# Kernel optimization log

Measured on AMD Instinct MI355X. Metric: run time of the kernel, lower is better.

## Reference

```python
import jax, jax.numpy as jnp
import numpy as np

B, S = 256, 256          # batch, seq_len
V, E = 8000, 128         # char vocab, char emb dim
HC, HW = 128, 256        # char_lstm_hid_dim, word_lstm_hid_dim


def setup_inputs() -> dict:
    key = jax.random.key(0)
    ks = jax.random.split(key, 20)
    n = lambda k, sh: (jax.random.normal(k, sh) * 0.05).astype(jnp.float32)
    return {
        "insts": jax.random.randint(ks[0], (B, S), 0, V),
        "golds": jax.random.randint(ks[1], (B, S), 0, 3),
        "emb": n(ks[2], (V, E)),
        "Wih_f": n(ks[3], (4 * HC, E)), "Whh_f": n(ks[4], (4 * HC, HC)), "b_f": n(ks[5], (4 * HC,)),
        "Wih_b": n(ks[6], (4 * HC, E)), "Whh_b": n(ks[7], (4 * HC, HC)), "b_b": n(ks[8], (4 * HC,)),
        "sub_Wih": n(ks[9], (4 * HW, 2 * HC)), "sub_Whh": n(ks[10], (4 * HW, HW)), "sub_b": n(ks[11], (4 * HW,)),
        "wrd_Wih": n(ks[12], (4 * HW, HW)), "wrd_Whh": n(ks[13], (4 * HW, HW)), "wrd_b": n(ks[14], (4 * HW,)),
        "cls_W": n(ks[15], (2, HW + 2 * HC)), "cls_b": n(ks[16], (2,)),
    }


def _cell(x, h, c, Wih, Whh, b):
    # PyTorch LSTMCell convention: gates ordered i, f, g, o
    g = x @ Wih.T + h @ Whh.T + b
    i, f, gg, o = jnp.split(g, 4, axis=-1)
    c = jax.nn.sigmoid(f) * c + jax.nn.sigmoid(i) * jnp.tanh(gg)
    h = jax.nn.sigmoid(o) * jnp.tanh(c)
    return h, c


def reference(insts, golds, emb, Wih_f, Whh_f, b_f, Wih_b, Whh_b, b_b,
              sub_Wih, sub_Whh, sub_b, wrd_Wih, wrd_Whh, wrd_b, cls_W, cls_b):
    # --- CharEncoder: embedding + BiLSTM, seq-first output [S, B, 2*HC] ---
    x = emb[insts].transpose(1, 0, 2)  # [S, B, E]
    z = jnp.zeros((B, HC), x.dtype)

    def mk_step(Wih, Whh, b):
        def step(hc, xt):
            h, c = _cell(xt, hc[0], hc[1], Wih, Whh, b)
            return (h, c), h
        return step

    _, hf = jax.lax.scan(mk_step(Wih_f, Whh_f, b_f), (z, z), x)
    _, hb = jax.lax.scan(mk_step(Wih_b, Whh_b, b_b), (z, z), x[::-1])
    chars = jnp.concatenate([hf, hb[::-1]], axis=-1)  # [S, B, 2*HC]

    # subword LSTM input at step t is chars[t-1] (zeros at t=0)
    sub_in = jnp.concatenate([jnp.zeros((1, B, 2 * HC), chars.dtype), chars[:-1]], axis=0)

    smap = jnp.array([1, 2, 2], jnp.int32)  # subword_action_map
    wmap = jnp.array([0, 1, 1], jnp.int32)  # word_action_map
    bidx = jnp.arange(B)

    # stacks: read state at pos, write new state at pos+1, then pos += op
    sh = jnp.zeros((2 * S + 2, B, HW), chars.dtype)
    sc = jnp.zeros((2 * S + 2, B, HW), chars.dtype)
    wh = jnp.zeros((S + 1, B, HW), chars.dtype)
    wc = jnp.zeros((S + 1, B, HW), chars.dtype)
    sp = jnp.zeros((B,), jnp.int32)
    wp = jnp.zeros((B,), jnp.int32)

    def step(carry, inp):
        sh, sc, sp, wh, wc, wp = carry
        xs, xc, g = inp  # subword input [B,2HC], classifier char feat [B,2HC], gold op [B]
        h1, c1 = _cell(xs, sh[sp, bidx], sc[sp, bidx], sub_Wih, sub_Whh, sub_b)
        sh = sh.at[sp + 1, bidx].set(h1)
        sc = sc.at[sp + 1, bidx].set(c1)
        h2, c2 = _cell(h1, wh[wp, bidx], wc[wp, bidx], wrd_Wih, wrd_Whh, wrd_b)
        wh = wh.at[wp + 1, bidx].set(h2)
        wc = wc.at[wp + 1, bidx].set(c2)
        out = jnp.concatenate([h2, xc], axis=-1) @ cls_W.T + cls_b  # [B, 2]
        return (sh, sc, sp + smap[g], wh, wc, wp + wmap[g]), out

    _, outs = jax.lax.scan(step, (sh, sc, sp, wh, wc, wp),
                           (sub_in, chars, golds.T.astype(jnp.int32)))
    return outs.transpose(1, 0, 2)  # [B, S, 2]
```

## Files before the change

### kernel.cpp

```cpp
#include <hip/hip_runtime.h>

#define S_LEN 256
#define BATCH 256

typedef _Float16 f16;
typedef _Float16 f16x8 __attribute__((ext_vector_type(8)));
typedef _Float16 f16x4 __attribute__((ext_vector_type(4)));
typedef float f32x4 __attribute__((ext_vector_type(4)));
typedef unsigned u32x4 __attribute__((ext_vector_type(4)));

__device__ inline float sigf(float x) { return 1.f / (1.f + __expf(-x)); }
__device__ inline float tanhf2(float x) { return 2.f * sigf(2.f * x) - 1.f; }

#define BARRIER_LGKM() asm volatile("s_waitcnt lgkmcnt(0)\n\ts_barrier" ::: "memory")

__global__ void k_convert(const float* __restrict__ w3, const float* __restrict__ w4,
                          const float* __restrict__ w6, const float* __restrict__ w7,
                          const float* __restrict__ w9, const float* __restrict__ w10,
                          const float* __restrict__ w12, const float* __restrict__ w13,
                          f16* __restrict__ dst) {
  int i = blockIdx.x * blockDim.x + threadIdx.x;
  const int n = 1310720;
  for (; i < n; i += gridDim.x * blockDim.x) {
    float v;
    if (i < 262144) {
      int m = i >> 16, j = i & 65535;
      v = (m == 0 ? w3 : m == 1 ? w4 : m == 2 ? w6 : w7)[j];
    } else {
      int k = i - 262144;
      int m = k >> 18, j = k & 262143;
      v = (m == 0 ? w9 : m == 1 ? w10 : m == 2 ? w12 : w13)[j];
    }
    dst[i] = (f16)v;
  }
}

__global__ void k_zero(unsigned* __restrict__ p, int n) {
  int i = blockIdx.x * blockDim.x + threadIdx.x;
  for (; i < n; i += gridDim.x * blockDim.x) p[i] = 0u;
}

__global__ void k_gather(const int* __restrict__ insts, const float* __restrict__ emb,
                         f16* __restrict__ Xf) {
  int gid = blockIdx.x * blockDim.x + threadIdx.x;
  int row = gid >> 5;
  int ch = gid & 31;
  int t = row >> 8, b = row & 255;
  int v = insts[b * S_LEN + t];
  const float* src = emb + (size_t)v * 128 + ch * 4;
  f16x4 d;
  d[0] = (f16)src[0]; d[1] = (f16)src[1]; d[2] = (f16)src[2]; d[3] = (f16)src[3];
  *(f16x4*)&Xf[(size_t)row * 128 + ch * 4] = d;
}

__global__ __launch_bounds__(512, 2)
void k_char_fused(const f16* __restrict__ wbuf, const float* __restrict__ bias_f,
                  const float* __restrict__ bias_b, const f16* __restrict__ Xf,
                  f16* __restrict__ chars) {
  const int dr = blockIdx.x >> 6;
  const int slice = blockIdx.x & 63;
  const int teamc = slice >> 2;
  const f16* Wih = wbuf + (dr ? 131072 : 0);
  const f16* Whh = wbuf + (dr ? 196608 : 65536);
  const float* bias = dr ? bias_b : bias_f;
  const int tid = threadIdx.x, lane = tid & 63, wave = tid >> 6;
  const int l15 = lane & 15, kb = (lane >> 4) * 8;
  const int bq = lane >> 4;
  const int u0 = wave * 16;
  const int cbase = dr ? 128 : 0;
  const int xrow = (slice * 4 + l15 < 256) ? (slice * 4 + l15) : 255;

  __shared__ f16 hs[2][16][136];
  __shared__ float gex[4][512];

  f16x8 fw[4][4], fh[4][4];
  float bv[4];
#pragma unroll
  for (int g = 0; g < 4; ++g) {
    const int row = g * 128 + u0 + l15;
    bv[g] = bias[row];
#pragma unroll
    for (int ks = 0; ks < 4; ++ks) {
      fw[g][ks] = *(const f16x8*)&Wih[row * 128 + ks * 32 + kb];
      fh[g][ks] = *(const f16x8*)&Whh[row * 128 + ks * 32 + kb];
    }
  }

  for (int i = tid; i < 2 * 16 * 136; i += 512) ((f16*)hs)[i] = (f16)0.f;
  __syncthreads();

  const int cb = tid >> 7;
  const int cu = tid & 127;
  float c = 0.f;

  f32x4 gacc[4];
  {
    const int t0 = dr ? 255 : 0;
    f16x8 ax[4];
#pragma unroll
    for (int ks = 0; ks < 4; ++ks)
      ax[ks] = *(const f16x8*)&Xf[(size_t)t0 * BATCH * 128 + xrow * 128 + ks * 32 + kb];
#pragma unroll
    for (int g = 0; g < 4; ++g) { f32x4 a = {bv[g], bv[g], bv[g], bv[g]}; gacc[g] = a; }
#pragma unroll
    for (int ks = 0; ks < 4; ++ks)
#pragma unroll
      for (int g = 0; g < 4; ++g)
        gacc[g] = __builtin_amdgcn_mfma_f32_16x16x32_f16(ax[ks], fw[g][ks], gacc[g], 0, 0, 0);
  }

  int par = 0;
  for (int st = 0; st < 256; ++st) {
    f16x8 axn[4];
    if (st < 255) {
      const int tn = dr ? (254 - st) : (st + 1);
#pragma unroll
      for (int ks = 0; ks < 4; ++ks)
        axn[ks] = *(const f16x8*)&Xf[(size_t)tn * BATCH * 128 + xrow * 128 + ks * 32 + kb];
    }

    f16x8 ah[4];
#pragma unroll
    for (int ks = 0; ks < 4; ++ks) ah[ks] = *(const f16x8*)&hs[par][l15][ks * 32 + kb];
    f32x4 acc[4];
#pragma unroll
    for (int g = 0; g < 4; ++g) acc[g] = gacc[g];
#pragma unroll
    for (int ks = 0; ks < 4; ++ks)
#pragma unroll
      for (int g = 0; g < 4; ++g)
        acc[g] = __builtin_amdgcn_mfma_f32_16x16x32_f16(ah[ks], fh[g][ks], acc[g], 0, 0, 0);

    if (bq == 0) {
#pragma unroll
      for (int g = 0; g < 4; ++g)
#pragma unroll
        for (int r = 0; r < 4; ++r) gex[r][g * 128 + u0 + l15] = acc[g][r];
    }
    BARRIER_LGKM();

    {
      float gi = gex[cb][cu], gf = gex[cb][128 + cu], gg = gex[cb][256 + cu],
            go = gex[cb][384 + cu];
      float cc = sigf(gf) * c + sigf(gi) * tanhf2(gg);
      c = cc;
      f16 hv = (f16)(sigf(go) * tanhf2(cc));
      const int t_out = dr ? (255 - st) : st;
      const int gr = slice * 4 + cb;
      chars[((size_t)(teamc * 256 + t_out) * 16 + (gr & 15)) * 256 + cbase + cu] = hv;
      hs[par ^ 1][cb][cu] = hv;
    }

    if (st < 255) {
#pragma unroll
      for (int g = 0; g < 4; ++g) { f32x4 a = {bv[g], bv[g], bv[g], bv[g]}; gacc[g] = a; }
#pragma unroll
      for (int ks = 0; ks < 4; ++ks)
#pragma unroll
        for (int g = 0; g < 4; ++g)
          gacc[g] =
              __builtin_amdgcn_mfma_f32_16x16x32_f16(axn[ks], fw[g][ks], gacc[g], 0, 0, 0);
    }
    par ^= 1;
    BARRIER_LGKM();
  }
}

__global__ __launch_bounds__(256, 1)
void k_subword(const f16* __restrict__ wbuf, const f16* __restrict__ chars,
               const int* __restrict__ golds,
               const float* __restrict__ b_sub, const float* __restrict__ b_wrd,
               unsigned* __restrict__ pub, unsigned* __restrict__ flags,
               f16* __restrict__ H2) {
  const int team = blockIdx.x >> 4;
  const int q = blockIdx.x & 15;
  const int m0 = team * 16;
  const int h0 = q * 16;
  const int tid = threadIdx.x, lane = tid & 63, wave = tid >> 6;
  const int l15 = lane & 15, kb = (lane >> 4) * 8;

  const f16* sWih = wbuf + 262144;
  const f16* sWhh = wbuf + 524288;
  const f16* wWih = wbuf + 786432;
  const f16* wWhh = wbuf + 1048576;

  __shared__ f16 xs_s[16][264];
  __shared__ f16 h1_s[16][264];
  __shared__ f16 wh_s[16][264];
  __shared__ float gexS[16][68];
  __shared__ float gexW[16][68];
  __shared__ int golds_s[16][256];

  f32x4 fsi[8], fsh[8], fwi[8], fwh[8];
  const int wr = wave * 256 + h0 + l15;
#pragma unroll
  for (int ks = 0; ks < 8; ++ks) {
    fsi[ks] = *(const volatile f32x4*)&sWih[wr * 256 + ks * 32 + kb];
    fsh[ks] = *(const volatile f32x4*)&sWhh[wr * 256 + ks * 32 + kb];
    fwi[ks] = *(const volatile f32x4*)&wWih[wr * 256 + ks * 32 + kb];
    fwh[ks] = *(const volatile f32x4*)&wWhh[wr * 256 + ks * 32 + kb];
  }
  const float bS = b_sub[wr], bW = b_wrd[wr];

  for (int i = tid; i < 16 * 256; i += 256)
    golds_s[i >> 8][i & 255] = golds[(m0 + (i >> 8)) * S_LEN + (i & 255)];
  for (int i = tid; i < 16 * 264; i += 256) {
    ((f16*)xs_s)[i] = (f16)0.f;
    ((f16*)h1_s)[i] = (f16)0.f;
    ((f16*)wh_s)[i] = (f16)0.f;
  }
  const int cm = tid >> 4, cj = tid & 15;
  const int sr = tid >> 4;
  const int sc = (tid & 15) * 16;
  float c_sub = 0.f, c_wrd = 0.f, wh_reg = 0.f;
  __syncthreads();

  for (int i = 0; i <= S_LEN; ++i) {
    const bool doW = (i > 0), doS = (i < S_LEN);
    const int slotbase = ((i & 1) * 16 + team) << 12;

    f16x4 chpre[4];
    if (doS) {
#pragma unroll
      for (int p = 0; p < 4; ++p)
        chpre[p] = *(const f16x4*)&chars[(size_t)(((team * S_LEN + i) * 16 + sr) * 256) +
                                         sc + p * 4];
    }

    f32x4 accW = {bW, bW, bW, bW};
    f32x4 accS = {bS, bS, bS, bS};
    if (doW) {
#pragma unroll
      for (int ks = 0; ks < 8; ++ks) {
        f16x8 a1 = *(const f16x8*)&h1_s[l15][ks * 32 + kb];
        f16x8 aw = *(const f16x8*)&wh_s[l15][ks * 32 + kb];
        accW = __builtin_amdgcn_mfma_f32_16x16x32_f16(
            a1, __builtin_bit_cast(f16x8, fwi[ks]), accW, 0, 0, 0);
        accW = __builtin_amdgcn_mfma_f32_16x16x32_f16(
            aw, __builtin_bit_cast(f16x8, fwh[ks]), accW, 0, 0, 0);
      }
    }
    if (doS) {
      const bool keep = (i > 0) && (golds_s[l15][i > 0 ? i - 1 : 0] == 0);
      f16x8 z8 = {};
#pragma unroll
      for (int ks = 0; ks < 8; ++ks) {
        f16x8 axv = *(const f16x8*)&xs_s[l15][ks * 32 + kb];
        f16x8 a1 = *(const f16x8*)&h1_s[l15][ks * 32 + kb];
        a1 = keep ? a1 : z8;
        accS = __builtin_amdgcn_mfma_f32_16x16x32_f16(
            axv, __builtin_bit_cast(f16x8, fsi[ks]), accS, 0, 0, 0);
        accS = __builtin_amdgcn_mfma_f32_16x16x32_f16(
            a1, __builtin_bit_cast(f16x8, fsh[ks]), accS, 0, 0, 0);
      }
    }
#pragma unroll
    for (int r = 0; r < 4; ++r) {
      if (doW) gexW[(lane >> 4) * 4 + r][wave * 16 + l15] = accW[r];
      if (doS) gexS[(lane >> 4) * 4 + r][wave * 16 + l15] = accS[r];
    }
    __syncthreads();

    const int gprev = (i > 0) ? golds_s[cm][i - 1] : 1;
    if (doW) {
      float gi = gexW[cm][cj], gf = gexW[cm][16 + cj], gg = gexW[cm][32 + cj],
            go = gexW[cm][48 + cj];
      float c2 = sigf(gf) * c_wrd + sigf(gi) * tanhf2(gg);
      float h2 = sigf(go) * tanhf2(c2);
      bool adv = (gprev != 0);
      if (adv) { c_wrd = c2; wh_reg = h2; }
      H2[(size_t)(i - 1) * BATCH * 256 + (m0 + cm) * 256 + h0 + cj] = (f16)h2;
    }
    if (doS) {
      float gi = gexS[cm][cj], gf = gexS[cm][16 + cj], gg = gexS[cm][32 + cj],
            go = gexS[cm][48 + cj];
      float cp = (gprev == 0) ? c_sub : 0.f;
      float c1 = sigf(gf) * cp + sigf(gi) * tanhf2(gg);
      c_sub = c1;
      f16 h1 = (f16)(sigf(go) * tanhf2(c1));
      unsigned val = ((unsigned)__builtin_bit_cast(unsigned short, h1) << 16) |
                     (unsigned)__builtin_bit_cast(unsigned short, (f16)wh_reg);
      __hip_atomic_store(&pub[slotbase + cm * 256 + h0 + cj], val, __ATOMIC_RELAXED,
                         __HIP_MEMORY_SCOPE_AGENT);
    }
    __syncthreads();

    if (doS) {
      if (tid == 0)
        __hip_atomic_store(&flags[(team * 16 + q) * 16], (unsigned)(i + 1), __ATOMIC_RELAXED,
                           __HIP_MEMORY_SCOPE_AGENT);
      if (tid < 64) {
        const unsigned tgt = (unsigned)(i + 1);
        while (true) {
          unsigned v = tgt;
          if (lane < 16)
            v = __hip_atomic_load(&flags[(team * 16 + lane) * 16], __ATOMIC_RELAXED,
                                  __HIP_MEMORY_SCOPE_AGENT);
          if (__all(v >= tgt)) break;
          __builtin_amdgcn_s_sleep(1);
        }
      }
      asm volatile("" ::: "memory");
      __syncthreads();
      u32x4 w0, w1, w2, w3;
      {
        const unsigned* pb = &pub[slotbase + sr * 256 + sc];
        asm volatile(
            "global_load_dwordx4 %0, %4, off sc0 sc1\n\t"
            "global_load_dwordx4 %1, %5, off sc0 sc1\n\t"
            "global_load_dwordx4 %2, %6, off sc0 sc1\n\t"
            "global_load_dwordx4 %3, %7, off sc0 sc1\n\t"
            "s_waitcnt vmcnt(0)"
            : "=&v"(w0), "=&v"(w1), "=&v"(w2), "=&v"(w3)
            : "v"(pb), "v"(pb + 4), "v"(pb + 8), "v"(pb + 12));
      }
      union { unsigned short s[8]; f16x8 v; } uh0, uw0, uh1, uw1;
#pragma unroll
      for (int k = 0; k < 4; ++k) {
        uh0.s[k] = (unsigned short)(w0[k] >> 16);
        uw0.s[k] = (unsigned short)(w0[k] & 0xffffu);
        uh0.s[4 + k] = (unsigned short)(w1[k] >> 16);
        uw0.s[4 + k] = (unsigned short)(w1[k] & 0xffffu);
        uh1.s[k] = (unsigned short)(w2[k] >> 16);
        uw1.s[k] = (unsigned short)(w2[k] & 0xffffu);
        uh1.s[4 + k] = (unsigned short)(w3[k] >> 16);
        uw1.s[4 + k] = (unsigned short)(w3[k] & 0xffffu);
      }
      *(f16x8*)&h1_s[sr][sc] = uh0.v;
      *(f16x8*)&wh_s[sr][sc] = uw0.v;
      *(f16x8*)&h1_s[sr][sc + 8] = uh1.v;
      *(f16x8*)&wh_s[sr][sc + 8] = uw1.v;
#pragma unroll
      for (int p = 0; p < 4; ++p) *(f16x4*)&xs_s[sr][sc + p * 4] = chpre[p];
      __syncthreads();
    }
  }
}

__global__ __launch_bounds__(256)
void k_cls(const f16* __restrict__ H2, const f16* __restrict__ chars,
           const float* __restrict__ clsW, const float* __restrict__ clsb,
           float* __restrict__ out) {
  const int w = (blockIdx.x << 2) | (threadIdx.x >> 6);
  const int lane = threadIdx.x & 63;
  const int t = w >> 8, b = w & 255;
  const f16* h2p = H2 + (size_t)w * 256;
  const f16* chp = chars + (size_t)(((b >> 4) * S_LEN + t) * 16 + (b & 15)) * 256;
  float s0 = 0.f, s1 = 0.f;
  f16x4 hv = *(const f16x4*)&h2p[lane * 4];
  f16x4 cv = *(const f16x4*)&chp[lane * 4];
#pragma unroll
  for (int qq = 0; qq < 4; ++qq) {
    int u = lane * 4 + qq;
    s0 += (float)hv[qq] * clsW[u] + (float)cv[qq] * clsW[256 + u];
    s1 += (float)hv[qq] * clsW[512 + u] + (float)cv[qq] * clsW[768 + u];
  }
#pragma unroll
  for (int off = 32; off >= 1; off >>= 1) {
    s0 += __shfl_down(s0, off);
    s1 += __shfl_down(s1, off);
  }
  if (lane == 0) {
    out[((size_t)b * S_LEN + t) * 2 + 0] = s0 + clsb[0];
    out[((size_t)b * S_LEN + t) * 2 + 1] = s1 + clsb[1];
  }
}

extern "C" void kernel_launch(void* const* d_in, const int* in_sizes, int n_in,
                              void* d_out, int out_size, void* d_ws, size_t ws_size,
                              hipStream_t stream) {
  const int* insts = (const int*)d_in[0];
  const int* golds = (const int*)d_in[1];
  const float* emb = (const float*)d_in[2];
  const float* wihf = (const float*)d_in[3];
  const float* whhf = (const float*)d_in[4];
  const float* bf = (const float*)d_in[5];
  const float* wihb = (const float*)d_in[6];
  const float* whhb = (const float*)d_in[7];
  const float* bb = (const float*)d_in[8];
  const float* swih = (const float*)d_in[9];
  const float* swhh = (const float*)d_in[10];
  const float* sb = (const float*)d_in[11];
  const float* wwih = (const float*)d_in[12];
  const float* wwhh = (const float*)d_in[13];
  const float* wb = (const float*)d_in[14];
  const float* clsW = (const float*)d_in[15];
  const float* clsb = (const float*)d_in[16];
  float* out = (float*)d_out;

  const size_t OFF_W = 0;
  const size_t OFF_XF = 2621440;
  const size_t OFF_PUB = OFF_XF + 4194304;
  const size_t OFF_FLAGS = OFF_PUB + 524288;
  const size_t OFF_CHARS = 19398656;
  const size_t OFF_A = 52953088;
  const size_t TOTAL = 87048192;
  if (ws_size < TOTAL) return;

  char* ws = (char*)d_ws;
  f16* wbuf = (f16*)(ws + OFF_W);
  f16* Xf = (f16*)(ws + OFF_XF);
  f16* chars = (f16*)(ws + OFF_CHARS);
  f16* H2 = (f16*)(ws + OFF_A);
  unsigned* pub = (unsigned*)(ws + OFF_PUB);
  unsigned* flags = (unsigned*)(ws + OFF_FLAGS);

  hipLaunchKernelGGL(k_convert, dim3(1024), dim3(256), 0, stream, wihf, whhf, wihb, whhb,
                     swih, swhh, wwih, wwhh, wbuf);
  hipLaunchKernelGGL(k_gather, dim3(8192), dim3(256), 0, stream, insts, emb, Xf);

  hipLaunchKernelGGL(k_char_fused, dim3(128), dim3(512), 0, stream, wbuf, bf, bb, Xf, chars);

  hipLaunchKernelGGL(k_zero, dim3(16), dim3(256), 0, stream, (unsigned*)(ws + OFF_FLAGS),
                     4096);
  hipLaunchKernelGGL(k_subword, dim3(256), dim3(256), 0, stream, wbuf, chars, golds, sb, wb,
                     pub, flags, H2);
  hipLaunchKernelGGL(k_cls, dim3(16384), dim3(256), 0, stream, H2, chars, clsW, clsb, out);
}
```

Baseline: 1.207 ms.

## Tag published subword state with step number and prefetch before flag spin

```diff
diff --git a/kernel.cpp b/kernel.cpp
--- a/kernel.cpp
+++ b/kernel.cpp
@@ -170,7 +170,7 @@
 void k_subword(const f16* __restrict__ wbuf, const f16* __restrict__ chars,
                const int* __restrict__ golds,
                const float* __restrict__ b_sub, const float* __restrict__ b_wrd,
-               unsigned* __restrict__ pub, unsigned* __restrict__ flags,
+               unsigned long long* __restrict__ pub, unsigned* __restrict__ flags,
                f16* __restrict__ H2) {
   const int team = blockIdx.x >> 4;
   const int q = blockIdx.x & 15;
@@ -278,8 +278,9 @@
       float c1 = sigf(gf) * cp + sigf(gi) * tanhf2(gg);
       c_sub = c1;
       f16 h1 = (f16)(sigf(go) * tanhf2(c1));
-      unsigned val = ((unsigned)__builtin_bit_cast(unsigned short, h1) << 16) |
-                     (unsigned)__builtin_bit_cast(unsigned short, (f16)wh_reg);
+      unsigned data = ((unsigned)__builtin_bit_cast(unsigned short, h1) << 16) |
+                      (unsigned)__builtin_bit_cast(unsigned short, (f16)wh_reg);
+      unsigned long long val = ((unsigned long long)(i + 1) << 32) | (unsigned long long)data;
       __hip_atomic_store(&pub[slotbase + cm * 256 + h0 + cj], val, __ATOMIC_RELAXED,
                          __HIP_MEMORY_SCOPE_AGENT);
     }
@@ -289,6 +290,21 @@
       if (tid == 0)
         __hip_atomic_store(&flags[(team * 16 + q) * 16], (unsigned)(i + 1), __ATOMIC_RELAXED,
                            __HIP_MEMORY_SCOPE_AGENT);
+      u32x4 w0, w1, w2, w3, w4, w5, w6, w7;
+      const unsigned long long* pb = &pub[slotbase + sr * 256 + sc];
+      asm volatile(
+          "global_load_dwordx4 %0, %8, off sc0 sc1\n\t"
+          "global_load_dwordx4 %1, %9, off sc0 sc1\n\t"
+          "global_load_dwordx4 %2, %10, off sc0 sc1\n\t"
+          "global_load_dwordx4 %3, %11, off sc0 sc1\n\t"
+          "global_load_dwordx4 %4, %12, off sc0 sc1\n\t"
+          "global_load_dwordx4 %5, %13, off sc0 sc1\n\t"
+          "global_load_dwordx4 %6, %14, off sc0 sc1\n\t"
+          "global_load_dwordx4 %7, %15, off sc0 sc1"
+          : "=&v"(w0), "=&v"(w1), "=&v"(w2), "=&v"(w3), "=&v"(w4), "=&v"(w5), "=&v"(w6),
+            "=&v"(w7)
+          : "v"(pb), "v"(pb + 2), "v"(pb + 4), "v"(pb + 6), "v"(pb + 8), "v"(pb + 10),
+            "v"(pb + 12), "v"(pb + 14));
       if (tid < 64) {
         const unsigned tgt = (unsigned)(i + 1);
         while (true) {
@@ -302,30 +318,44 @@
       }
       asm volatile("" ::: "memory");
       __syncthreads();
-      u32x4 w0, w1, w2, w3;
+      asm volatile("s_waitcnt vmcnt(0)"
+                   : "+v"(w0), "+v"(w1), "+v"(w2), "+v"(w3), "+v"(w4), "+v"(w5), "+v"(w6),
+                     "+v"(w7)
+                   :
+                   : "memory");
       {
-        const unsigned* pb = &pub[slotbase + sr * 256 + sc];
-        asm volatile(
-            "global_load_dwordx4 %0, %4, off sc0 sc1\n\t"
-            "global_load_dwordx4 %1, %5, off sc0 sc1\n\t"
-            "global_load_dwordx4 %2, %6, off sc0 sc1\n\t"
-            "global_load_dwordx4 %3, %7, off sc0 sc1\n\t"
-            "s_waitcnt vmcnt(0)"
-            : "=&v"(w0), "=&v"(w1), "=&v"(w2), "=&v"(w3)
-            : "v"(pb), "v"(pb + 4), "v"(pb + 8), "v"(pb + 12));
+        const unsigned tgt = (unsigned)(i + 1);
+        unsigned bad = (w0[1] ^ tgt) | (w0[3] ^ tgt) | (w1[1] ^ tgt) | (w1[3] ^ tgt) |
+                       (w2[1] ^ tgt) | (w2[3] ^ tgt) | (w3[1] ^ tgt) | (w3[3] ^ tgt) |
+                       (w4[1] ^ tgt) | (w4[3] ^ tgt) | (w5[1] ^ tgt) | (w5[3] ^ tgt) |
+                       (w6[1] ^ tgt) | (w6[3] ^ tgt) | (w7[1] ^ tgt) | (w7[3] ^ tgt);
+        if (bad) {
+          asm volatile(
+              "global_load_dwordx4 %0, %8, off sc0 sc1\n\t"
+              "global_load_dwordx4 %1, %9, off sc0 sc1\n\t"
+              "global_load_dwordx4 %2, %10, off sc0 sc1\n\t"
+              "global_load_dwordx4 %3, %11, off sc0 sc1\n\t"
+              "global_load_dwordx4 %4, %12, off sc0 sc1\n\t"
+              "global_load_dwordx4 %5, %13, off sc0 sc1\n\t"
+              "global_load_dwordx4 %6, %14, off sc0 sc1\n\t"
+              "global_load_dwordx4 %7, %15, off sc0 sc1\n\t"
+              "s_waitcnt vmcnt(0)"
+              : "=&v"(w0), "=&v"(w1), "=&v"(w2), "=&v"(w3), "=&v"(w4), "=&v"(w5), "=&v"(w6),
+                "=&v"(w7)
+              : "v"(pb), "v"(pb + 2), "v"(pb + 4), "v"(pb + 6), "v"(pb + 8), "v"(pb + 10),
+                "v"(pb + 12), "v"(pb + 14)
+              : "memory");
+        }
       }
       union { unsigned short s[8]; f16x8 v; } uh0, uw0, uh1, uw1;
-#pragma unroll
-      for (int k = 0; k < 4; ++k) {
-        uh0.s[k] = (unsigned short)(w0[k] >> 16);
-        uw0.s[k] = (unsigned short)(w0[k] & 0xffffu);
-        uh0.s[4 + k] = (unsigned short)(w1[k] >> 16);
-        uw0.s[4 + k] = (unsigned short)(w1[k] & 0xffffu);
-        uh1.s[k] = (unsigned short)(w2[k] >> 16);
-        uw1.s[k] = (unsigned short)(w2[k] & 0xffffu);
-        uh1.s[4 + k] = (unsigned short)(w3[k] >> 16);
-        uw1.s[4 + k] = (unsigned short)(w3[k] & 0xffffu);
-      }
+#define UNPK(W, UH, UW, o)                                     \
+  UH.s[o] = (unsigned short)(W[0] >> 16);                      \
+  UW.s[o] = (unsigned short)(W[0] & 0xffffu);                  \
+  UH.s[(o) + 1] = (unsigned short)(W[2] >> 16);                \
+  UW.s[(o) + 1] = (unsigned short)(W[2] & 0xffffu);
+      UNPK(w0, uh0, uw0, 0) UNPK(w1, uh0, uw0, 2) UNPK(w2, uh0, uw0, 4) UNPK(w3, uh0, uw0, 6)
+      UNPK(w4, uh1, uw1, 0) UNPK(w5, uh1, uw1, 2) UNPK(w6, uh1, uw1, 4) UNPK(w7, uh1, uw1, 6)
+#undef UNPK
       *(f16x8*)&h1_s[sr][sc] = uh0.v;
       *(f16x8*)&wh_s[sr][sc] = uw0.v;
       *(f16x8*)&h1_s[sr][sc + 8] = uh1.v;
@@ -391,7 +421,7 @@
   const size_t OFF_W = 0;
   const size_t OFF_XF = 2621440;
   const size_t OFF_PUB = OFF_XF + 4194304;
-  const size_t OFF_FLAGS = OFF_PUB + 524288;
+  const size_t OFF_FLAGS = OFF_PUB + 1048576;
   const size_t OFF_CHARS = 19398656;
   const size_t OFF_A = 52953088;
   const size_t TOTAL = 87048192;
@@ -402,7 +432,7 @@
   f16* Xf = (f16*)(ws + OFF_XF);
   f16* chars = (f16*)(ws + OFF_CHARS);
   f16* H2 = (f16*)(ws + OFF_A);
-  unsigned* pub = (unsigned*)(ws + OFF_PUB);
+  unsigned long long* pub = (unsigned long long*)(ws + OFF_PUB);
   unsigned* flags = (unsigned*)(ws + OFF_FLAGS);
 
   hipLaunchKernelGGL(k_convert, dim3(1024), dim3(256), 0, stream, wihf, whhf, wihb, whhb,
```

Result: slower. 1.611 ms (+33.4%).
